# Kernel tuning notes

Hardware: AMD Instinct MI355X
Metric: run time of the kernel (lower is better)

Reference implementation:

```python
import jax, jax.numpy as jnp
import numpy as np

B, S, D = 2, 2048, 2048
H, HD = 16, 128


def _rope_cos_sin(seq_len, head_dim, base=10000.0):
    inv_freq = 1.0 / (base ** (np.arange(0, head_dim, 2, dtype=np.float32) / head_dim))
    t = np.arange(seq_len, dtype=np.float32)
    freqs = np.outer(t, inv_freq)                      # [S, HD/2]
    emb = np.concatenate([freqs, freqs], axis=-1)      # [S, HD]
    return jnp.asarray(np.cos(emb)), jnp.asarray(np.sin(emb))


def setup_inputs() -> dict:
    key = jax.random.key(0)
    k1, k2, k3 = jax.random.split(key, 3)
    hidden_states = jax.random.normal(k1, (B, S, D), dtype=jnp.float32)
    cos, sin = _rope_cos_sin(S, HD)
    # qkv weight: [3, H*HD, D] as in CastedLinear(batch_output_dims=(3,))
    w_qkv = jax.random.normal(k2, (3, H * HD, D), dtype=jnp.float32) * (1.0 / D ** 0.5)
    w_o = jax.random.normal(k3, (D, H * HD), dtype=jnp.float32) * (1.0 / (H * HD) ** 0.5)
    return {"hidden_states": hidden_states, "cos": cos, "sin": sin, "w_qkv": w_qkv, "w_o": w_o}


def _rotate_half(x):
    x1, x2 = jnp.split(x, 2, axis=-1)
    return jnp.concatenate([-x2, x1], axis=-1)


def _apply_rope(x, cos, sin):
    # x: [B, S, H, HD]; cos/sin: [S, HD] -> broadcast over heads via [:, None, :]
    return x * cos[:, None, :] + _rotate_half(x) * sin[:, None, :]


def reference(hidden_states, cos, sin, w_qkv, w_o):
    # fused QKV projection: weight flattened to [3*H*HD, D]
    qkv = jnp.einsum('bsd,fd->bsf', hidden_states, w_qkv.reshape(-1, D))  # [B,S,3*H*HD]
    # rearrange '... (h hd) -> ... h hd' with h=H  ->  [B,S,H,3*HD], then chunk
    qkv = qkv.reshape(B, S, H, 3 * HD)
    q, k, v = jnp.split(qkv, 3, axis=-1)          # each [B,S,H,HD]
    q = _apply_rope(q, cos, sin)
    k = _apply_rope(k, cos, sin)
    # SDPA, causal
    scale = 1.0 / jnp.sqrt(jnp.asarray(HD, dtype=q.dtype))
    scores = jnp.einsum('bshd,bthd->bhst', q, k) * scale      # [B,H,S,S]
    causal = jnp.tril(jnp.ones((S, S), dtype=bool))
    scores = jnp.where(causal, scores, jnp.asarray(-jnp.inf, dtype=scores.dtype))
    probs = jax.nn.softmax(scores, axis=-1)
    attn = jnp.einsum('bhst,bthd->bshd', probs, v)            # [B,S,H,HD]
    attn = attn.reshape(B, S, H * HD)
    return jnp.einsum('bsf,df->bsd', attn, w_o)               # [B,S,D]
```

## Files before the change

### kernel.cpp

```cpp
#include <hip/hip_runtime.h>

typedef unsigned short u16;
typedef __bf16 bf16x8 __attribute__((ext_vector_type(8)));
typedef float f32x4 __attribute__((ext_vector_type(4)));


__device__ __forceinline__ u16 f2bf(float x) {
  __bf16 h = (__bf16)x;
  return __builtin_bit_cast(u16, h);
}
__device__ __forceinline__ float bf2f(u16 u) {
  unsigned int v = ((unsigned int)u) << 16;
  return __builtin_bit_cast(float, v);
}

__device__ __forceinline__ void async_copy16(void* lds, const void* g) {
  __builtin_amdgcn_global_load_lds((const __attribute__((address_space(1))) void*)g,
                                   (__attribute__((address_space(3))) void*)lds, 16, 0, 0);
}

__global__ __launch_bounds__(256) void cast_f32_bf16(const float* __restrict__ src,
                                                     u16* __restrict__ dst, int n4) {
  int i = blockIdx.x * 256 + threadIdx.x;
  if (i >= n4) return;
  float4 v = ((const float4*)src)[i];
  ushort4 o;
  o.x = f2bf(v.x); o.y = f2bf(v.y); o.z = f2bf(v.z); o.w = f2bf(v.w);
  ((ushort4*)dst)[i] = o;
}

__global__ __launch_bounds__(256) void gemm_qkv(const u16* __restrict__ A,
                                                const u16* __restrict__ W,
                                                u16* __restrict__ Qb,
                                                u16* __restrict__ Kb,
                                                u16* __restrict__ Vt) {
  __shared__ __align__(16) u16 As[128 * 64];
  __shared__ __align__(16) u16 Bs[128 * 64];
  const int tid = threadIdx.x;
  const int lane = tid & 63;
  const int wave = tid >> 6;
  const int wm = (wave >> 1) * 64;
  const int wn = (wave & 1) * 64;
  const int r16 = lane & 15;
  const int g4 = lane >> 4;
  const int rsw = r16 & 7;
  const int bm = blockIdx.x * 128;
  const int bn = blockIdx.y * 128;

  size_t aoff[4], boff[4];
  u16* ldsA[4];
  u16* ldsB[4];
#pragma unroll
  for (int i = 0; i < 4; i++) {
    int row = wave * 32 + i * 8 + (lane >> 3);
    int c = (lane & 7) ^ (row & 7);
    aoff[i] = (size_t)(bm + row) * 2048 + c * 8;
    boff[i] = (size_t)(bn + row) * 2048 + c * 8;
    ldsA[i] = &As[(wave * 4 + i) * 512];
    ldsB[i] = &Bs[(wave * 4 + i) * 512];
  }

  f32x4 acc[4][4];
  f32x4 zero = {0.0f, 0.0f, 0.0f, 0.0f};
#pragma unroll
  for (int m = 0; m < 4; m++)
#pragma unroll
    for (int n = 0; n < 4; n++) acc[m][n] = zero;

  for (int kt = 0; kt < 2048; kt += 64) {
    __syncthreads();
#pragma unroll
    for (int i = 0; i < 4; i++) {
      async_copy16(ldsA[i], A + aoff[i] + kt);
      async_copy16(ldsB[i], W + boff[i] + kt);
    }
    __syncthreads();
#pragma unroll
    for (int ks = 0; ks < 2; ks++) {
      bf16x8 af[4], bfr[4];
#pragma unroll
      for (int m = 0; m < 4; m++)
        af[m] = *(const bf16x8*)(&As[(wm + m * 16 + r16) * 64 + ((ks * 4 + g4) ^ rsw) * 8]);
#pragma unroll
      for (int n = 0; n < 4; n++)
        bfr[n] = *(const bf16x8*)(&Bs[(wn + n * 16 + r16) * 64 + ((ks * 4 + g4) ^ rsw) * 8]);
#pragma unroll
      for (int m = 0; m < 4; m++)
#pragma unroll
        for (int n = 0; n < 4; n++)
          acc[m][n] = __builtin_amdgcn_mfma_f32_16x16x32_bf16(af[m], bfr[n], acc[m][n], 0, 0, 0);
    }
  }

  const int which = blockIdx.y % 3;
  const int hh = blockIdx.y / 3;
#pragma unroll
  for (int m = 0; m < 4; m++) {
#pragma unroll
    for (int n = 0; n < 4; n++) {
#pragma unroll
      for (int r = 0; r < 4; r++) {
        int row = bm + wm + m * 16 + g4 * 4 + r;
        int hd = wn + n * 16 + r16;
        int bb = row >> 11;
        int s = row & 2047;
        size_t bhIdx = (size_t)(bb * 16 + hh);
        u16 o = f2bf(acc[m][n][r]);
        if (which == 2)
          Vt[(bhIdx * 128 + hd) * 2048 + s] = o;
        else if (which == 1)
          Kb[(bhIdx * 2048 + s) * 128 + hd] = o;
        else
          Qb[(bhIdx * 2048 + s) * 128 + hd] = o;
      }
    }
  }
}

__global__ __launch_bounds__(256) void rope_kernel(u16* __restrict__ Qb, u16* __restrict__ Kb,
                                                   const float* __restrict__ cosb,
                                                   const float* __restrict__ sinb) {
  int id = blockIdx.x * 256 + threadIdx.x;
  int j = id & 15;
  int s = (id >> 4) & 2047;
  int bh = (id >> 15) & 31;
  int tt = id >> 20;
  u16* row = (tt ? Kb : Qb) + ((size_t)bh * 2048 + s) * 128;
  int i = j * 4;
  float4 c = *(const float4*)(cosb + s * 128 + i);
  float4 sn = *(const float4*)(sinb + s * 128 + i);
  ushort4 a = *(ushort4*)(row + i);
  ushort4 b = *(ushort4*)(row + 64 + i);
  float x10 = bf2f(a.x), x11 = bf2f(a.y), x12 = bf2f(a.z), x13 = bf2f(a.w);
  float x20 = bf2f(b.x), x21 = bf2f(b.y), x22 = bf2f(b.z), x23 = bf2f(b.w);
  ushort4 o1, o2;
  o1.x = f2bf(x10 * c.x - x20 * sn.x);
  o1.y = f2bf(x11 * c.y - x21 * sn.y);
  o1.z = f2bf(x12 * c.z - x22 * sn.z);
  o1.w = f2bf(x13 * c.w - x23 * sn.w);
  o2.x = f2bf(x20 * c.x + x10 * sn.x);
  o2.y = f2bf(x21 * c.y + x11 * sn.y);
  o2.z = f2bf(x22 * c.z + x12 * sn.z);
  o2.w = f2bf(x23 * c.w + x13 * sn.w);
  *(ushort4*)(row + i) = o1;
  *(ushort4*)(row + 64 + i) = o2;
}

__global__ __launch_bounds__(256) void flash_attn(const u16* __restrict__ Q,
                                                  const u16* __restrict__ K,
                                                  const u16* __restrict__ Vt,
                                                  u16* __restrict__ O) {
  __shared__ __align__(16) u16 Ks[64 * 128];
  __shared__ __align__(16) u16 Vs[128 * 64];
  __shared__ __align__(16) u16 Ps[4 * 16 * 72];
  const int tid = threadIdx.x;
  const int lane = tid & 63;
  const int wave = tid >> 6;
  const int bh = blockIdx.y;
  const int r16 = lane & 15;
  const int g4 = lane >> 4;
  const int rsw = r16 & 7;
  const u16* Qh = Q + (size_t)bh * 2048 * 128;
  const u16* Kh = K + (size_t)bh * 2048 * 128;
  const u16* Vh = Vt + (size_t)bh * 128 * 2048;
  const int b = bh >> 4;
  const int h = bh & 15;

  int krow = (wave * 4 + 0) * 4 + (lane >> 4);
  size_t koff[4], voff[4];
  u16* ldsK[4];
  u16* ldsV[4];
#pragma unroll
  for (int i = 0; i < 4; i++) {
    int kr = (wave * 4 + i) * 4 + (lane >> 4);
    int kc = (lane & 15) ^ (kr & 7);
    koff[i] = (size_t)kr * 128 + kc * 8;
    ldsK[i] = &Ks[(wave * 4 + i) * 512];
    int vr = (wave * 4 + i) * 8 + (lane >> 3);
    int vc = (lane & 7) ^ (vr & 7);
    voff[i] = (size_t)vr * 2048 + vc * 8;
    ldsV[i] = &Vs[(wave * 4 + i) * 512];
  }
  (void)krow;

  const float sc = 0.08838834764831845f * 1.4426950408889634f;

#pragma unroll 1
  for (int pass = 0; pass < 2; pass++) {
    const int t = pass == 0 ? (int)blockIdx.x : 31 - (int)blockIdx.x;

    bf16x8 qf[4];
    {
      int qrow = t * 64 + wave * 16 + r16;
#pragma unroll
      for (int ks = 0; ks < 4; ks++)
        qf[ks] = *(const bf16x8*)(Qh + (size_t)qrow * 128 + ks * 32 + g4 * 8);
    }

    f32x4 o[8];
    f32x4 zero = {0.0f, 0.0f, 0.0f, 0.0f};
#pragma unroll
    for (int c = 0; c < 8; c++) o[c] = zero;
    float m_i[4], l_i[4];
#pragma unroll
    for (int r = 0; r < 4; r++) { m_i[r] = -__builtin_inff(); l_i[r] = 0.0f; }

    for (int u = 0; u <= t; u++) {
      __syncthreads();
#pragma unroll
      for (int i = 0; i < 4; i++) {
        async_copy16(ldsK[i], Kh + (size_t)u * 64 * 128 + koff[i]);
        async_copy16(ldsV[i], Vh + (size_t)u * 64 + voff[i]);
      }
      __syncthreads();

      f32x4 sacc[4];
#pragma unroll
      for (int n = 0; n < 4; n++) sacc[n] = zero;
#pragma unroll
      for (int n = 0; n < 4; n++) {
#pragma unroll
        for (int ks = 0; ks < 4; ks++) {
          bf16x8 kf = *(const bf16x8*)(&Ks[(n * 16 + r16) * 128 + ((ks * 4 + g4) ^ rsw) * 8]);
          sacc[n] = __builtin_amdgcn_mfma_f32_16x16x32_bf16(qf[ks], kf, sacc[n], 0, 0, 0);
        }
      }

      float p[4][4];
      float alpha[4];
#pragma unroll
      for (int r = 0; r < 4; r++) {
        int rowg = t * 64 + wave * 16 + g4 * 4 + r;
        float e[4];
#pragma unroll
        for (int n = 0; n < 4; n++) {
          e[n] = sacc[n][r] * sc;
          if (u == t) {
            int key = u * 64 + n * 16 + r16;
            if (key > rowg) e[n] = -__builtin_inff();
          }
        }
        float mr = fmaxf(fmaxf(e[0], e[1]), fmaxf(e[2], e[3]));
        mr = fmaxf(mr, __shfl_xor(mr, 1));
        mr = fmaxf(mr, __shfl_xor(mr, 2));
        mr = fmaxf(mr, __shfl_xor(mr, 4));
        mr = fmaxf(mr, __shfl_xor(mr, 8));
        float mn = fmaxf(m_i[r], mr);
        alpha[r] = exp2f(m_i[r] - mn);
        m_i[r] = mn;
        float srow = 0.0f;
#pragma unroll
        for (int n = 0; n < 4; n++) {
          float pv = exp2f(e[n] - mn);
          p[n][r] = pv;
          srow += pv;
        }
        srow += __shfl_xor(srow, 1);
        srow += __shfl_xor(srow, 2);
        srow += __shfl_xor(srow, 4);
        srow += __shfl_xor(srow, 8);
        l_i[r] = l_i[r] * alpha[r] + srow;
      }
#pragma unroll
      for (int c = 0; c < 8; c++)
#pragma unroll
        for (int r = 0; r < 4; r++) o[c][r] *= alpha[r];

      u16* Pw = &Ps[wave * 16 * 72];
#pragma unroll
      for (int n = 0; n < 4; n++)
#pragma unroll
        for (int r = 0; r < 4; r++)
          Pw[(g4 * 4 + r) * 72 + n * 16 + r16] = f2bf(p[n][r]);

#pragma unroll
      for (int ks2 = 0; ks2 < 2; ks2++) {
        bf16x8 pf = *(const bf16x8*)(&Pw[r16 * 72 + ks2 * 32 + g4 * 8]);
#pragma unroll
        for (int c = 0; c < 8; c++) {
          bf16x8 vf = *(const bf16x8*)(&Vs[(c * 16 + r16) * 64 + ((ks2 * 4 + g4) ^ rsw) * 8]);
          o[c] = __builtin_amdgcn_mfma_f32_16x16x32_bf16(pf, vf, o[c], 0, 0, 0);
        }
      }
    }

    float rl[4];
#pragma unroll
    for (int r = 0; r < 4; r++) rl[r] = 1.0f / l_i[r];
#pragma unroll
    for (int c = 0; c < 8; c++) {
#pragma unroll
      for (int r = 0; r < 4; r++) {
        int rowg = t * 64 + wave * 16 + g4 * 4 + r;
        int col = c * 16 + r16;
        O[((size_t)(b * 2048 + rowg)) * 2048 + h * 128 + col] = f2bf(o[c][r] * rl[r]);
      }
    }
  }
}

__global__ __launch_bounds__(256) void gemm_out(const u16* __restrict__ A,
                                                const u16* __restrict__ W,
                                                float* __restrict__ out) {
  __shared__ __align__(16) u16 As[128 * 64];
  __shared__ __align__(16) u16 Bs[128 * 64];
  const int tid = threadIdx.x;
  const int lane = tid & 63;
  const int wave = tid >> 6;
  const int wm = (wave >> 1) * 64;
  const int wn = (wave & 1) * 64;
  const int r16 = lane & 15;
  const int g4 = lane >> 4;
  const int rsw = r16 & 7;
  const int bm = blockIdx.x * 128;
  const int bn = blockIdx.y * 128;

  size_t aoff[4], boff[4];
  u16* ldsA[4];
  u16* ldsB[4];
#pragma unroll
  for (int i = 0; i < 4; i++) {
    int row = wave * 32 + i * 8 + (lane >> 3);
    int c = (lane & 7) ^ (row & 7);
    aoff[i] = (size_t)(bm + row) * 2048 + c * 8;
    boff[i] = (size_t)(bn + row) * 2048 + c * 8;
    ldsA[i] = &As[(wave * 4 + i) * 512];
    ldsB[i] = &Bs[(wave * 4 + i) * 512];
  }

  f32x4 acc[4][4];
  f32x4 zero = {0.0f, 0.0f, 0.0f, 0.0f};
#pragma unroll
  for (int m = 0; m < 4; m++)
#pragma unroll
    for (int n = 0; n < 4; n++) acc[m][n] = zero;

  for (int kt = 0; kt < 2048; kt += 64) {
    __syncthreads();
#pragma unroll
    for (int i = 0; i < 4; i++) {
      async_copy16(ldsA[i], A + aoff[i] + kt);
      async_copy16(ldsB[i], W + boff[i] + kt);
    }
    __syncthreads();
#pragma unroll
    for (int ks = 0; ks < 2; ks++) {
      bf16x8 af[4], bfr[4];
#pragma unroll
      for (int m = 0; m < 4; m++)
        af[m] = *(const bf16x8*)(&As[(wm + m * 16 + r16) * 64 + ((ks * 4 + g4) ^ rsw) * 8]);
#pragma unroll
      for (int n = 0; n < 4; n++)
        bfr[n] = *(const bf16x8*)(&Bs[(wn + n * 16 + r16) * 64 + ((ks * 4 + g4) ^ rsw) * 8]);
#pragma unroll
      for (int m = 0; m < 4; m++)
#pragma unroll
        for (int n = 0; n < 4; n++)
          acc[m][n] = __builtin_amdgcn_mfma_f32_16x16x32_bf16(af[m], bfr[n], acc[m][n], 0, 0, 0);
    }
  }

#pragma unroll
  for (int m = 0; m < 4; m++) {
#pragma unroll
    for (int n = 0; n < 4; n++) {
#pragma unroll
      for (int r = 0; r < 4; r++) {
        int row = bm + wm + m * 16 + g4 * 4 + r;
        int col = bn + wn + n * 16 + r16;
        out[(size_t)row * 2048 + col] = acc[m][n][r];
      }
    }
  }
}

extern "C" void kernel_launch(void* const* d_in, const int* in_sizes, int n_in,
                              void* d_out, int out_size, void* d_ws, size_t ws_size,
                              hipStream_t stream) {
  const float* hidden = (const float*)d_in[0];
  const float* cosb   = (const float*)d_in[1];
  const float* sinb   = (const float*)d_in[2];
  const float* w_qkv  = (const float*)d_in[3];
  const float* w_o    = (const float*)d_in[4];
  float* out = (float*)d_out;

  char* ws = (char*)d_ws;
  u16* Xbf    = (u16*)(ws);
  u16* Wqkvbf = (u16*)(ws + 16777216);
  u16* Wobf   = (u16*)(ws + 41943040);
  u16* Qb     = (u16*)(ws + 50331648);
  u16* Kb     = (u16*)(ws + 67108864);
  u16* Vt     = (u16*)(ws + 83886080);
  u16* Ob     = (u16*)(ws + 100663296);

  cast_f32_bf16<<<8192, 256, 0, stream>>>(hidden, Xbf, 2097152);
  cast_f32_bf16<<<12288, 256, 0, stream>>>(w_qkv, Wqkvbf, 3145728);
  cast_f32_bf16<<<4096, 256, 0, stream>>>(w_o, Wobf, 1048576);
  gemm_qkv<<<dim3(32, 48), 256, 0, stream>>>(Xbf, Wqkvbf, Qb, Kb, Vt);
  rope_kernel<<<8192, 256, 0, stream>>>(Qb, Kb, cosb, sinb);
  flash_attn<<<dim3(16, 32), 256, 0, stream>>>(Qb, Kb, Vt, Ob);
  gemm_out<<<dim3(32, 16), 256, 0, stream>>>(Ob, Wobf, out);
}
```

Before: 445.3 us.

## Fuse casts, fold RoPE into QKV epilogue, double-buffer and transpose flash attention

Merges the three cast launches into one kernel and applies RoPE inside the QKV GEMM epilogue by remapping wave column tiles so each thread holds both rotate-half partners, which removes the separate rope pass over Q and K. Flash attention double-buffers the K/V tiles in LDS so the next tile loads while the current one is computed, dropping one barrier per iteration. It also computes S transposed (K as the A operand), so each lane owns one query row and softmax reductions need only two cross-lane shuffles. The costs are twice the LDS for K/V, extra shuffles to hand alpha and l back to the output layout, and scattered 2-byte stores of the P tile to LDS.

```diff
diff --git a/kernel.cpp b/kernel.cpp
--- a/kernel.cpp
+++ b/kernel.cpp
@@ -9,28 +9,35 @@
   __bf16 h = (__bf16)x;
   return __builtin_bit_cast(u16, h);
 }
-__device__ __forceinline__ float bf2f(u16 u) {
-  unsigned int v = ((unsigned int)u) << 16;
-  return __builtin_bit_cast(float, v);
-}
 
 __device__ __forceinline__ void async_copy16(void* lds, const void* g) {
   __builtin_amdgcn_global_load_lds((const __attribute__((address_space(1))) void*)g,
                                    (__attribute__((address_space(3))) void*)lds, 16, 0, 0);
 }
 
-__global__ __launch_bounds__(256) void cast_f32_bf16(const float* __restrict__ src,
-                                                     u16* __restrict__ dst, int n4) {
+__global__ __launch_bounds__(256) void cast_all(const float* __restrict__ hidden,
+                                                const float* __restrict__ wqkv,
+                                                const float* __restrict__ wo,
+                                                u16* __restrict__ xb,
+                                                u16* __restrict__ wqb,
+                                                u16* __restrict__ wob) {
   int i = blockIdx.x * 256 + threadIdx.x;
-  if (i >= n4) return;
-  float4 v = ((const float4*)src)[i];
+  const float* s;
+  u16* d;
+  int off;
+  if (i < 2097152) { s = hidden; d = xb; off = i; }
+  else if (i < 2097152 + 3145728) { s = wqkv; d = wqb; off = i - 2097152; }
+  else { s = wo; d = wob; off = i - (2097152 + 3145728); }
+  float4 v = ((const float4*)s)[off];
   ushort4 o;
   o.x = f2bf(v.x); o.y = f2bf(v.y); o.z = f2bf(v.z); o.w = f2bf(v.w);
-  ((ushort4*)dst)[i] = o;
+  ((ushort4*)d)[off] = o;
 }
 
 __global__ __launch_bounds__(256) void gemm_qkv(const u16* __restrict__ A,
                                                 const u16* __restrict__ W,
+                                                const float* __restrict__ cosb,
+                                                const float* __restrict__ sinb,
                                                 u16* __restrict__ Qb,
                                                 u16* __restrict__ Kb,
                                                 u16* __restrict__ Vt) {
@@ -40,7 +47,6 @@
   const int lane = tid & 63;
   const int wave = tid >> 6;
   const int wm = (wave >> 1) * 64;
-  const int wn = (wave & 1) * 64;
   const int r16 = lane & 15;
   const int g4 = lane >> 4;
   const int rsw = r16 & 7;
@@ -60,6 +66,10 @@
     ldsB[i] = &Bs[(wave * 4 + i) * 512];
   }
 
+  int bcol[4];
+#pragma unroll
+  for (int n = 0; n < 4; n++) bcol[n] = (wave & 1) * 32 + (n & 1) * 16 + (n >> 1) * 64;
+
   f32x4 acc[4][4];
   f32x4 zero = {0.0f, 0.0f, 0.0f, 0.0f};
 #pragma unroll
@@ -83,7 +93,7 @@
         af[m] = *(const bf16x8*)(&As[(wm + m * 16 + r16) * 64 + ((ks * 4 + g4) ^ rsw) * 8]);
 #pragma unroll
       for (int n = 0; n < 4; n++)
-        bfr[n] = *(const bf16x8*)(&Bs[(wn + n * 16 + r16) * 64 + ((ks * 4 + g4) ^ rsw) * 8]);
+        bfr[n] = *(const bf16x8*)(&Bs[(bcol[n] + r16) * 64 + ((ks * 4 + g4) ^ rsw) * 8]);
 #pragma unroll
       for (int m = 0; m < 4; m++)
 #pragma unroll
@@ -97,61 +107,39 @@
 #pragma unroll
   for (int m = 0; m < 4; m++) {
 #pragma unroll
-    for (int n = 0; n < 4; n++) {
-#pragma unroll
-      for (int r = 0; r < 4; r++) {
-        int row = bm + wm + m * 16 + g4 * 4 + r;
-        int hd = wn + n * 16 + r16;
-        int bb = row >> 11;
-        int s = row & 2047;
-        size_t bhIdx = (size_t)(bb * 16 + hh);
-        u16 o = f2bf(acc[m][n][r]);
-        if (which == 2)
-          Vt[(bhIdx * 128 + hd) * 2048 + s] = o;
-        else if (which == 1)
-          Kb[(bhIdx * 2048 + s) * 128 + hd] = o;
-        else
-          Qb[(bhIdx * 2048 + s) * 128 + hd] = o;
-      }
-    }
-  }
-}
-
-__global__ __launch_bounds__(256) void rope_kernel(u16* __restrict__ Qb, u16* __restrict__ Kb,
-                                                   const float* __restrict__ cosb,
-                                                   const float* __restrict__ sinb) {
-  int id = blockIdx.x * 256 + threadIdx.x;
-  int j = id & 15;
-  int s = (id >> 4) & 2047;
-  int bh = (id >> 15) & 31;
-  int tt = id >> 20;
-  u16* row = (tt ? Kb : Qb) + ((size_t)bh * 2048 + s) * 128;
-  int i = j * 4;
-  float4 c = *(const float4*)(cosb + s * 128 + i);
-  float4 sn = *(const float4*)(sinb + s * 128 + i);
-  ushort4 a = *(ushort4*)(row + i);
-  ushort4 b = *(ushort4*)(row + 64 + i);
-  float x10 = bf2f(a.x), x11 = bf2f(a.y), x12 = bf2f(a.z), x13 = bf2f(a.w);
-  float x20 = bf2f(b.x), x21 = bf2f(b.y), x22 = bf2f(b.z), x23 = bf2f(b.w);
-  ushort4 o1, o2;
-  o1.x = f2bf(x10 * c.x - x20 * sn.x);
-  o1.y = f2bf(x11 * c.y - x21 * sn.y);
-  o1.z = f2bf(x12 * c.z - x22 * sn.z);
-  o1.w = f2bf(x13 * c.w - x23 * sn.w);
-  o2.x = f2bf(x20 * c.x + x10 * sn.x);
-  o2.y = f2bf(x21 * c.y + x11 * sn.y);
-  o2.z = f2bf(x22 * c.z + x12 * sn.z);
-  o2.w = f2bf(x23 * c.w + x13 * sn.w);
-  *(ushort4*)(row + i) = o1;
-  *(ushort4*)(row + 64 + i) = o2;
+    for (int r = 0; r < 4; r++) {
+      int row = bm + wm + m * 16 + g4 * 4 + r;
+      int bb = row >> 11;
+      int s = row & 2047;
+      size_t bhIdx = (size_t)(bb * 16 + hh);
+      if (which == 2) {
+#pragma unroll
+        for (int n = 0; n < 4; n++) {
+          int hd = bcol[n] + r16;
+          Vt[(bhIdx * 128 + hd) * 2048 + s] = f2bf(acc[m][n][r]);
+        }
+      } else {
+        u16* dst = (which ? Kb : Qb) + (bhIdx * 2048 + s) * 128;
+#pragma unroll
+        for (int n = 0; n < 2; n++) {
+          int hd = bcol[n] + r16;
+          float c = cosb[s * 128 + hd];
+          float sn = sinb[s * 128 + hd];
+          float x1 = acc[m][n][r], x2 = acc[m][n + 2][r];
+          dst[hd] = f2bf(x1 * c - x2 * sn);
+          dst[hd + 64] = f2bf(x2 * c + x1 * sn);
+        }
+      }
+    }
+  }
 }
 
 __global__ __launch_bounds__(256) void flash_attn(const u16* __restrict__ Q,
                                                   const u16* __restrict__ K,
                                                   const u16* __restrict__ Vt,
                                                   u16* __restrict__ O) {
-  __shared__ __align__(16) u16 Ks[64 * 128];
-  __shared__ __align__(16) u16 Vs[128 * 64];
+  __shared__ __align__(16) u16 Ks[2][64 * 128];
+  __shared__ __align__(16) u16 Vs[2][128 * 64];
   __shared__ __align__(16) u16 Ps[4 * 16 * 72];
   const int tid = threadIdx.x;
   const int lane = tid & 63;
@@ -166,22 +154,18 @@
   const int b = bh >> 4;
   const int h = bh & 15;
 
-  int krow = (wave * 4 + 0) * 4 + (lane >> 4);
   size_t koff[4], voff[4];
-  u16* ldsK[4];
-  u16* ldsV[4];
+  int ldsOff[4];
 #pragma unroll
   for (int i = 0; i < 4; i++) {
     int kr = (wave * 4 + i) * 4 + (lane >> 4);
     int kc = (lane & 15) ^ (kr & 7);
     koff[i] = (size_t)kr * 128 + kc * 8;
-    ldsK[i] = &Ks[(wave * 4 + i) * 512];
     int vr = (wave * 4 + i) * 8 + (lane >> 3);
     int vc = (lane & 7) ^ (vr & 7);
     voff[i] = (size_t)vr * 2048 + vc * 8;
-    ldsV[i] = &Vs[(wave * 4 + i) * 512];
-  }
-  (void)krow;
+    ldsOff[i] = (wave * 4 + i) * 512;
+  }
 
   const float sc = 0.08838834764831845f * 1.4426950408889634f;
 
@@ -201,18 +185,26 @@
     f32x4 zero = {0.0f, 0.0f, 0.0f, 0.0f};
 #pragma unroll
     for (int c = 0; c < 8; c++) o[c] = zero;
-    float m_i[4], l_i[4];
-#pragma unroll
-    for (int r = 0; r < 4; r++) { m_i[r] = -__builtin_inff(); l_i[r] = 0.0f; }
-
+    float m_i = -__builtin_inff();
+    float l_i = 0.0f;
+
+    __syncthreads();
+#pragma unroll
+    for (int i = 0; i < 4; i++) {
+      async_copy16(&Ks[0][ldsOff[i]], Kh + koff[i]);
+      async_copy16(&Vs[0][ldsOff[i]], Vh + voff[i]);
+    }
+
+    int cur = 0;
     for (int u = 0; u <= t; u++) {
       __syncthreads();
-#pragma unroll
-      for (int i = 0; i < 4; i++) {
-        async_copy16(ldsK[i], Kh + (size_t)u * 64 * 128 + koff[i]);
-        async_copy16(ldsV[i], Vh + (size_t)u * 64 + voff[i]);
-      }
-      __syncthreads();
+      if (u < t) {
+#pragma unroll
+        for (int i = 0; i < 4; i++) {
+          async_copy16(&Ks[cur ^ 1][ldsOff[i]], Kh + (size_t)(u + 1) * 64 * 128 + koff[i]);
+          async_copy16(&Vs[cur ^ 1][ldsOff[i]], Vh + (size_t)(u + 1) * 64 + voff[i]);
+        }
+      }
 
       f32x4 sacc[4];
 #pragma unroll
@@ -221,72 +213,68 @@
       for (int n = 0; n < 4; n++) {
 #pragma unroll
         for (int ks = 0; ks < 4; ks++) {
-          bf16x8 kf = *(const bf16x8*)(&Ks[(n * 16 + r16) * 128 + ((ks * 4 + g4) ^ rsw) * 8]);
-          sacc[n] = __builtin_amdgcn_mfma_f32_16x16x32_bf16(qf[ks], kf, sacc[n], 0, 0, 0);
-        }
-      }
-
-      float p[4][4];
-      float alpha[4];
-#pragma unroll
-      for (int r = 0; r < 4; r++) {
-        int rowg = t * 64 + wave * 16 + g4 * 4 + r;
-        float e[4];
-#pragma unroll
-        for (int n = 0; n < 4; n++) {
-          e[n] = sacc[n][r] * sc;
+          bf16x8 kf = *(const bf16x8*)(&Ks[cur][(n * 16 + r16) * 128 + ((ks * 4 + g4) ^ rsw) * 8]);
+          sacc[n] = __builtin_amdgcn_mfma_f32_16x16x32_bf16(kf, qf[ks], sacc[n], 0, 0, 0);
+        }
+      }
+
+      const int qg = t * 64 + wave * 16 + r16;
+      float e[4][4];
+      float vmax = -__builtin_inff();
+#pragma unroll
+      for (int n = 0; n < 4; n++)
+#pragma unroll
+        for (int r = 0; r < 4; r++) {
+          float ev = sacc[n][r] * sc;
           if (u == t) {
-            int key = u * 64 + n * 16 + r16;
-            if (key > rowg) e[n] = -__builtin_inff();
+            int key = u * 64 + 16 * n + g4 * 4 + r;
+            if (key > qg) ev = -__builtin_inff();
           }
-        }
-        float mr = fmaxf(fmaxf(e[0], e[1]), fmaxf(e[2], e[3]));
-        mr = fmaxf(mr, __shfl_xor(mr, 1));
-        mr = fmaxf(mr, __shfl_xor(mr, 2));
-        mr = fmaxf(mr, __shfl_xor(mr, 4));
-        mr = fmaxf(mr, __shfl_xor(mr, 8));
-        float mn = fmaxf(m_i[r], mr);
-        alpha[r] = exp2f(m_i[r] - mn);
-        m_i[r] = mn;
-        float srow = 0.0f;
-#pragma unroll
-        for (int n = 0; n < 4; n++) {
-          float pv = exp2f(e[n] - mn);
-          p[n][r] = pv;
-          srow += pv;
-        }
-        srow += __shfl_xor(srow, 1);
-        srow += __shfl_xor(srow, 2);
-        srow += __shfl_xor(srow, 4);
-        srow += __shfl_xor(srow, 8);
-        l_i[r] = l_i[r] * alpha[r] + srow;
-      }
+          e[n][r] = ev;
+          vmax = fmaxf(vmax, ev);
+        }
+      vmax = fmaxf(vmax, __shfl_xor(vmax, 16));
+      vmax = fmaxf(vmax, __shfl_xor(vmax, 32));
+      float mn = fmaxf(m_i, vmax);
+      float alpha = exp2f(m_i - mn);
+      m_i = mn;
+      float ssum = 0.0f;
+      u16* Pw = &Ps[wave * 16 * 72];
+#pragma unroll
+      for (int n = 0; n < 4; n++)
+#pragma unroll
+        for (int r = 0; r < 4; r++) {
+          float pv = exp2f(e[n][r] - mn);
+          ssum += pv;
+          Pw[r16 * 72 + 16 * n + g4 * 4 + r] = f2bf(pv);
+        }
+      ssum += __shfl_xor(ssum, 16);
+      ssum += __shfl_xor(ssum, 32);
+      l_i = l_i * alpha + ssum;
+
+      float alpha_o[4];
+#pragma unroll
+      for (int r = 0; r < 4; r++) alpha_o[r] = __shfl(alpha, g4 * 4 + r);
 #pragma unroll
       for (int c = 0; c < 8; c++)
 #pragma unroll
-        for (int r = 0; r < 4; r++) o[c][r] *= alpha[r];
-
-      u16* Pw = &Ps[wave * 16 * 72];
-#pragma unroll
-      for (int n = 0; n < 4; n++)
-#pragma unroll
-        for (int r = 0; r < 4; r++)
-          Pw[(g4 * 4 + r) * 72 + n * 16 + r16] = f2bf(p[n][r]);
+        for (int r = 0; r < 4; r++) o[c][r] *= alpha_o[r];
 
 #pragma unroll
       for (int ks2 = 0; ks2 < 2; ks2++) {
         bf16x8 pf = *(const bf16x8*)(&Pw[r16 * 72 + ks2 * 32 + g4 * 8]);
 #pragma unroll
         for (int c = 0; c < 8; c++) {
-          bf16x8 vf = *(const bf16x8*)(&Vs[(c * 16 + r16) * 64 + ((ks2 * 4 + g4) ^ rsw) * 8]);
+          bf16x8 vf = *(const bf16x8*)(&Vs[cur][(c * 16 + r16) * 64 + ((ks2 * 4 + g4) ^ rsw) * 8]);
           o[c] = __builtin_amdgcn_mfma_f32_16x16x32_bf16(pf, vf, o[c], 0, 0, 0);
         }
       }
+      cur ^= 1;
     }
 
     float rl[4];
 #pragma unroll
-    for (int r = 0; r < 4; r++) rl[r] = 1.0f / l_i[r];
+    for (int r = 0; r < 4; r++) rl[r] = 1.0f / __shfl(l_i, g4 * 4 + r);
 #pragma unroll
     for (int c = 0; c < 8; c++) {
 #pragma unroll
@@ -393,11 +381,8 @@
   u16* Vt     = (u16*)(ws + 83886080);
   u16* Ob     = (u16*)(ws + 100663296);
 
-  cast_f32_bf16<<<8192, 256, 0, stream>>>(hidden, Xbf, 2097152);
-  cast_f32_bf16<<<12288, 256, 0, stream>>>(w_qkv, Wqkvbf, 3145728);
-  cast_f32_bf16<<<4096, 256, 0, stream>>>(w_o, Wobf, 1048576);
-  gemm_qkv<<<dim3(32, 48), 256, 0, stream>>>(Xbf, Wqkvbf, Qb, Kb, Vt);
-  rope_kernel<<<8192, 256, 0, stream>>>(Qb, Kb, cosb, sinb);
+  cast_all<<<24576, 256, 0, stream>>>(hidden, w_qkv, w_o, Xbf, Wqkvbf, Wobf);
+  gemm_qkv<<<dim3(32, 48), 256, 0, stream>>>(Xbf, Wqkvbf, cosb, sinb, Qb, Kb, Vt);
   flash_attn<<<dim3(16, 32), 256, 0, stream>>>(Qb, Kb, Vt, Ob);
   gemm_out<<<dim3(32, 16), 256, 0, stream>>>(Ob, Wobf, out);
 }
```

Result: faster. 411.1 us (-7.7%).
